# Performance work log

Hardware: AMD Instinct MI355X
Metric: run time of the kernel (lower is better)

## Reference

```python
import jax, jax.numpy as jnp
import numpy as np

N, IN_DIM, EDGE_DIM = 100000, 64, 16
E = 1600000
H, C = 4, 16  # heads, out_dim per head; H*C = 64
K = 3
NEG_SLOPE = 0.2
LN_EPS = 1e-5


def setup_inputs() -> dict:
    key = jax.random.key(0)
    ks = jax.random.split(key, 16)
    s = 1.0 / np.sqrt(IN_DIM)
    se = 1.0 / np.sqrt(EDGE_DIM)
    HC = H * C
    return {
        "x": jax.random.normal(ks[0], (N, IN_DIM), jnp.float32),
        "edge_index": jax.random.randint(ks[1], (2, E), 0, N, jnp.int32),
        "edge_attr": jax.random.normal(ks[2], (E, EDGE_DIM), jnp.float32),
        "dist_to_boundary": jax.random.randint(ks[3], (N,), 0, K + 1, jnp.int32),
        # GATv2Conv params
        "W_l": jax.random.normal(ks[4], (IN_DIM, HC), jnp.float32) * s,
        "b_l": jnp.zeros((HC,), jnp.float32),
        "W_r": jax.random.normal(ks[5], (IN_DIM, HC), jnp.float32) * s,
        "b_r": jnp.zeros((HC,), jnp.float32),
        "W_e": jax.random.normal(ks[6], (EDGE_DIM, HC), jnp.float32) * se,
        "att": jax.random.normal(ks[7], (H, C), jnp.float32) * (1.0 / np.sqrt(C)),
        "bias": jnp.zeros((HC,), jnp.float32),
        # LayerNorm params
        "gamma": jnp.ones((HC,), jnp.float32),
        "beta": jnp.zeros((HC,), jnp.float32),
        # residual: in_dim == H*C -> Identity in original; identity-initialized Linear
        "W_res": jnp.eye(IN_DIM, HC, dtype=jnp.float32),
        "b_res": jnp.zeros((HC,), jnp.float32),
        "bias_per_hop": jnp.zeros((K + 1,), jnp.float32),
    }


def reference(x, edge_index, edge_attr, dist_to_boundary,
              W_l, b_l, W_r, b_r, W_e, att, bias,
              gamma, beta, W_res, b_res, bias_per_hop):
    n = x.shape[0]
    src, dst = edge_index[0], edge_index[1]

    # hop bias on edge features (module indexes edge_index[1])
    hop = jnp.clip(dist_to_boundary[dst], 0, K)
    ea = edge_attr + bias_per_hop[hop][:, None] * 0.1  # [E, edge_dim]

    # GATv2Conv (eval mode: no dropout)
    xl = (x @ W_l + b_l).reshape(n, H, C)
    xr = (x @ W_r + b_r).reshape(n, H, C)
    ee = (ea @ W_e).reshape(-1, H, C)
    m = xl[src] + xr[dst] + ee                      # [E,H,C]
    m = jnp.where(m > 0, m, NEG_SLOPE * m)          # leaky_relu
    logits = jnp.einsum('ehc,hc->eh', m, att)       # [E,H]

    # segment softmax over destination nodes
    amax = jax.ops.segment_max(logits, dst, num_segments=n)
    ex = jnp.exp(logits - amax[dst])
    den = jax.ops.segment_sum(ex, dst, num_segments=n)
    alpha = ex / (den[dst] + 1e-16)                 # [E,H]

    # weighted scatter-add of source features
    out = jax.ops.segment_sum(alpha[:, :, None] * xl[src], dst, num_segments=n)
    out = out.reshape(n, H * C) + bias

    # LayerNorm
    mu = out.mean(-1, keepdims=True)
    var = ((out - mu) ** 2).mean(-1, keepdims=True)
    out = (out - mu) / jnp.sqrt(var + LN_EPS) * gamma + beta

    # residual (Identity in original since in_dim == H*C; W_res is identity)
    return out + (x @ W_res + b_res)
```

## Files before the change

kernel.cpp:

```cpp
#include <hip/hip_runtime.h>
#include <math.h>

#define NEG_SLOPE 0.2f
#define LN_EPS 1e-5f
#define BUCKET 48

typedef __attribute__((ext_vector_type(2))) float f32x2;

template <int CTRL>
__device__ __forceinline__ float dpp_add(float x) {
    int s = __builtin_amdgcn_update_dpp(0, __float_as_int(x), CTRL, 0xF, 0xF, true);
    return x + __int_as_float(s);
}
__device__ __forceinline__ float row16_sum(float x) {
    x = dpp_add<0xB1>(x);
    x = dpp_add<0x4E>(x);
    x = dpp_add<0x124>(x);
    x = dpp_add<0x128>(x);
    return x;
}

__global__ __launch_bounds__(256) void prep(
    const float* __restrict__ x,
    const float* __restrict__ W_l, const float* __restrict__ b_l,
    const float* __restrict__ W_r, const float* __restrict__ b_r,
    const float* __restrict__ W_res, const float* __restrict__ b_res,
    const float* __restrict__ W_e,
    const int* __restrict__ dist, const float* __restrict__ bph,
    float* __restrict__ xl, float* __restrict__ xr, float* __restrict__ xres_out,
    const int* __restrict__ ei, int* __restrict__ counts, int2* __restrict__ bucket,
    int n, int E_) {
    __shared__ float sWl[4096];
    __shared__ float sWr[4096];
    __shared__ float sWs[4096];
    __shared__ float sx[256];
    for (int i = threadIdx.x; i < 4096; i += 256) {
        sWl[i] = W_l[i]; sWr[i] = W_r[i]; sWs[i] = W_res[i];
    }
    int lane = threadIdx.x & 63;
    int w = threadIdx.x >> 6;
    float bl = b_l[lane], br = b_r[lane], bs = b_res[lane];
    float wsum = 0.0f;
#pragma unroll
    for (int k = 0; k < 16; ++k) wsum += W_e[k * 64 + lane];
    __syncthreads();
    for (int base = blockIdx.x * 4; base < n; base += gridDim.x * 4) {
        __syncthreads();
        int r = base + w;
        if (r < n) sx[threadIdx.x] = x[(size_t)r * 64 + lane];
        __syncthreads();
        if (r < n) {
            float al = bl, ar = br, as_ = bs;
            const float* xv = &sx[w * 64];
#pragma unroll
            for (int k = 0; k < 64; ++k) {
                float xk = xv[k];
                al = fmaf(xk, sWl[k * 64 + lane], al);
                ar = fmaf(xk, sWr[k * 64 + lane], ar);
                as_ = fmaf(xk, sWs[k * 64 + lane], as_);
            }
            int hop = dist[r];
            hop = hop < 0 ? 0 : (hop > 3 ? 3 : hop);
            float hb = 0.1f * bph[hop];
            xl[(size_t)r * 64 + lane] = al;
            xr[(size_t)r * 64 + lane] = fmaf(hb, wsum, ar);
            xres_out[(size_t)r * 64 + lane] = as_;
        }
    }
    const int* di = ei + E_;
    for (int e = blockIdx.x * 256 + threadIdx.x; e < E_; e += gridDim.x * 256) {
        int dst = di[e];
        int src = ei[e];
        int pos = atomicAdd(&counts[dst], 1);
        pos = pos < BUCKET - 1 ? pos : BUCKET - 1;
        bucket[(size_t)dst * BUCKET + pos] = make_int2(e, src);
    }
}

#define LOAD_G(G, EA)                                                       \
    {                                                                       \
        int ec = __builtin_amdgcn_readfirstlane((EA).x);                    \
        const f32x2* p = (const f32x2*)(eattr + (size_t)ec * 16);           \
        _Pragma("unroll") for (int k = 0; k < 8; ++k) G[k] = p[k];          \
    }

#define PHASE(G, X, E, DEN, ACC, I)                                         \
    {                                                                       \
        f32x2 mm; mm.x = X + base; mm.y = 0.0f;                             \
        _Pragma("unroll") for (int k = 0; k < 8; ++k)                       \
            mm = __builtin_elementwise_fma(G[k], w2[k], mm);                \
        float m = mm.x + mm.y;                                              \
        m = fmaxf(m, NEG_SLOPE * m);                                        \
        float l = row16_sum(m * attv);      \
        l = (I) < cnt ? l : -1e30f;                                         \
        float ex = __builtin_amdgcn_exp2f(l);                               \
        DEN += ex;                                                          \
        ACC = fmaf(ex, X, ACC);                                             \
        X = xl[((unsigned)(E).y << 6) | lane];                              \
        LOAD_G(G, E);                                                       \
        int nx = (I) + 6; nx = nx > last ? last : nx;                       \
        E = bk[nx];                                                         \
    }

__global__ __launch_bounds__(256) void fused_gather(
    const int* __restrict__ counts, const int2* __restrict__ bucket,
    const float* __restrict__ eattr,
    const float* __restrict__ W_e, const float* __restrict__ att,
    const float* __restrict__ xl, const float* __restrict__ xr,
    const float* __restrict__ bias,
    const float* __restrict__ gamma, const float* __restrict__ beta,
    float* out, int n) {
    int lane = threadIdx.x & 63;
    float attv = att[lane] * 1.44269504f;
    float bi = bias[lane], g = gamma[lane], be = beta[lane];
    f32x2 w2[8];
#pragma unroll
    for (int k = 0; k < 8; ++k) {
        w2[k].x = W_e[(2 * k) * 64 + lane];
        w2[k].y = W_e[(2 * k + 1) * 64 + lane];
    }

    int wid = (blockIdx.x * blockDim.x + threadIdx.x) >> 6;
    int nw = (gridDim.x * blockDim.x) >> 6;
    for (int r = wid; r < n; r += nw) {
        int cnt = counts[r];
        float den0 = 0.0f, den1 = 0.0f, den2 = 0.0f;
        float acc0 = 0.0f, acc1 = 0.0f, acc2 = 0.0f;
        if (cnt > 0) {
            cnt = cnt < BUCKET ? cnt : BUCKET;
            float base = xr[((unsigned)r << 6) | lane];
            const int2* bk = bucket + (size_t)r * BUCKET;
            int last = cnt - 1;
            int i1 = 1 > last ? last : 1;
            int i2 = 2 > last ? last : 2;
            int i3 = 3 > last ? last : 3;
            int i4 = 4 > last ? last : 4;
            int i5 = 5 > last ? last : 5;
            int2 A0 = bk[0];
            int2 A1 = bk[i1];
            int2 A2 = bk[i2];
            int2 E0 = bk[i3];
            int2 E1 = bk[i4];
            int2 E2 = bk[i5];
            float X0 = xl[((unsigned)A0.y << 6) | lane];
            float X1 = xl[((unsigned)A1.y << 6) | lane];
            float X2 = xl[((unsigned)A2.y << 6) | lane];
            f32x2 G0[8], G1[8], G2[8];
            LOAD_G(G0, A0);
            LOAD_G(G1, A1);
            LOAD_G(G2, A2);
            for (int i = 0; i < cnt; i += 3) {
                PHASE(G0, X0, E0, den0, acc0, i)
                PHASE(G1, X1, E1, den1, acc1, i + 1)
                PHASE(G2, X2, E2, den2, acc2, i + 2)
            }
        }
        float den = (den0 + den1) + den2;
        float acc = (acc0 + acc1) + acc2;
        float v = acc / (den + 1e-16f) + bi;
        float s = row16_sum(v);
        s += __shfl_xor(s, 16, 64);
        s += __shfl_xor(s, 32, 64);
        float mu = s * (1.0f / 64.0f);
        float dd = v - mu;
        float q = row16_sum(dd * dd);
        q += __shfl_xor(q, 16, 64);
        q += __shfl_xor(q, 32, 64);
        float var = q * (1.0f / 64.0f);
        float nv = dd * rsqrtf(var + LN_EPS) * g + be;
        unsigned idx = ((unsigned)r << 6) | lane;
        out[idx] = nv + out[idx];
    }
}

extern "C" void kernel_launch(void* const* d_in, const int* in_sizes, int n_in,
                              void* d_out, int out_size, void* d_ws, size_t ws_size,
                              hipStream_t stream) {
    const float* x     = (const float*)d_in[0];
    const int*   ei    = (const int*)d_in[1];
    const float* eattr = (const float*)d_in[2];
    const int*   dist  = (const int*)d_in[3];
    const float* W_l   = (const float*)d_in[4];
    const float* b_l   = (const float*)d_in[5];
    const float* W_r   = (const float*)d_in[6];
    const float* b_r   = (const float*)d_in[7];
    const float* W_e   = (const float*)d_in[8];
    const float* att   = (const float*)d_in[9];
    const float* bias  = (const float*)d_in[10];
    const float* gamma = (const float*)d_in[11];
    const float* beta  = (const float*)d_in[12];
    const float* W_res = (const float*)d_in[13];
    const float* b_res = (const float*)d_in[14];
    const float* bph   = (const float*)d_in[15];

    int n  = in_sizes[0] / 64;
    int E_ = in_sizes[1] / 2;
    float* out = (float*)d_out;

    char* ws = (char*)d_ws;
    float* xl     = (float*)ws; ws += (size_t)n * 64 * 4;
    float* xr     = (float*)ws; ws += (size_t)n * 64 * 4;
    int2*  bucket = (int2*)ws;  ws += (size_t)n * BUCKET * 8;
    int*   counts = (int*)ws;   ws += (size_t)n * 4;

    hipMemsetAsync(counts, 0, (size_t)n * 4, stream);
    prep<<<2048, 256, 0, stream>>>(x, W_l, b_l, W_r, b_r, W_res, b_res, W_e,
                                   dist, bph, xl, xr, out, ei, counts, bucket, n, E_);
    fused_gather<<<4096, 256, 0, stream>>>(counts, bucket, eattr,
                                           W_e, att, xl, xr,
                                           bias, gamma, beta, out, n);
}
```

Baseline: 279.8 us.

## Prefetch next row's bucket entries and counts across the gather loop

Restructures the per-wave row loop in fused_gather into a software pipeline. While the current destination row is processed, the next row's edge count, xr base and first six bucket entries are loaded in advance. Out-of-range prefetch slots are replaced with a valid entry instead of clamped indices. This is meant to hide the dependent counts → bucket → xl load chain at the start of each row. In exchange it holds more live registers and always issues some bucket loads even for low-degree rows.

```diff
diff --git a/kernel.cpp b/kernel.cpp
--- a/kernel.cpp
+++ b/kernel.cpp
@@ -92,7 +92,7 @@
         float m = mm.x + mm.y;                                              \
         m = fmaxf(m, NEG_SLOPE * m);                                        \
         float l = row16_sum(m * attv);      \
-        l = (I) < cnt ? l : -1e30f;                                         \
+        l = (I) < cc ? l : -1e30f;                                          \
         float ex = __builtin_amdgcn_exp2f(l);                               \
         DEN += ex;                                                          \
         ACC = fmaf(ex, X, ACC);                                             \
@@ -122,38 +122,51 @@
 
     int wid = (blockIdx.x * blockDim.x + threadIdx.x) >> 6;
     int nw = (gridDim.x * blockDim.x) >> 6;
-    for (int r = wid; r < n; r += nw) {
-        int cnt = counts[r];
+    if (wid >= n) return;
+    int r = wid;
+    int cnt = counts[r];
+    float base = xr[((unsigned)r << 6) | lane];
+    int2 A0, A1, A2, E0, E1, E2;
+    {
+        const int2* bkp = bucket + (size_t)r * BUCKET;
+        A0 = bkp[0]; A1 = bkp[1]; A2 = bkp[2];
+        E0 = bkp[3]; E1 = bkp[4]; E2 = bkp[5];
+    }
+    for (;;) {
+        const int2* bk = bucket + (size_t)r * BUCKET;
+        int cc = cnt < BUCKET ? cnt : BUCKET;
+        int last = cc - 1;
+        int2 Z = make_int2(0, 0);
+        A0 = cc > 0 ? A0 : Z;
+        A1 = last >= 1 ? A1 : A0;
+        A2 = last >= 2 ? A2 : A0;
+        E0 = last >= 3 ? E0 : A0;
+        E1 = last >= 4 ? E1 : A0;
+        E2 = last >= 5 ? E2 : A0;
+        float X0 = xl[((unsigned)A0.y << 6) | lane];
+        float X1 = xl[((unsigned)A1.y << 6) | lane];
+        float X2 = xl[((unsigned)A2.y << 6) | lane];
+        f32x2 G0[8], G1[8], G2[8];
+        LOAD_G(G0, A0);
+        LOAD_G(G1, A1);
+        LOAD_G(G2, A2);
+        int rn = r + nw;
+        int hn = rn < n;
+        int rc = hn ? rn : r;
+        int cntn = counts[rc];
+        float basen = xr[((unsigned)rc << 6) | lane];
+        int2 An0, An1, An2, En0, En1, En2;
+        {
+            const int2* bkn = bucket + (size_t)rc * BUCKET;
+            An0 = bkn[0]; An1 = bkn[1]; An2 = bkn[2];
+            En0 = bkn[3]; En1 = bkn[4]; En2 = bkn[5];
+        }
         float den0 = 0.0f, den1 = 0.0f, den2 = 0.0f;
         float acc0 = 0.0f, acc1 = 0.0f, acc2 = 0.0f;
-        if (cnt > 0) {
-            cnt = cnt < BUCKET ? cnt : BUCKET;
-            float base = xr[((unsigned)r << 6) | lane];
-            const int2* bk = bucket + (size_t)r * BUCKET;
-            int last = cnt - 1;
-            int i1 = 1 > last ? last : 1;
-            int i2 = 2 > last ? last : 2;
-            int i3 = 3 > last ? last : 3;
-            int i4 = 4 > last ? last : 4;
-            int i5 = 5 > last ? last : 5;
-            int2 A0 = bk[0];
-            int2 A1 = bk[i1];
-            int2 A2 = bk[i2];
-            int2 E0 = bk[i3];
-            int2 E1 = bk[i4];
-            int2 E2 = bk[i5];
-            float X0 = xl[((unsigned)A0.y << 6) | lane];
-            float X1 = xl[((unsigned)A1.y << 6) | lane];
-            float X2 = xl[((unsigned)A2.y << 6) | lane];
-            f32x2 G0[8], G1[8], G2[8];
-            LOAD_G(G0, A0);
-            LOAD_G(G1, A1);
-            LOAD_G(G2, A2);
-            for (int i = 0; i < cnt; i += 3) {
-                PHASE(G0, X0, E0, den0, acc0, i)
-                PHASE(G1, X1, E1, den1, acc1, i + 1)
-                PHASE(G2, X2, E2, den2, acc2, i + 2)
-            }
+        for (int i = 0; i < cc; i += 3) {
+            PHASE(G0, X0, E0, den0, acc0, i)
+            PHASE(G1, X1, E1, den1, acc1, i + 1)
+            PHASE(G2, X2, E2, den2, acc2, i + 2)
         }
         float den = (den0 + den1) + den2;
         float acc = (acc0 + acc1) + acc2;
@@ -170,6 +183,10 @@
         float nv = dd * rsqrtf(var + LN_EPS) * g + be;
         unsigned idx = ((unsigned)r << 6) | lane;
         out[idx] = nv + out[idx];
+        if (!hn) break;
+        r = rn; cnt = cntn; base = basen;
+        A0 = An0; A1 = An1; A2 = An2;
+        E0 = En0; E1 = En1; E2 = En2;
     }
 }
 
```

Measured after the change: 251.7 us, median of 2. 10.0% less time.
